# Performance work log

Measured on AMD Instinct MI355X. Metric: run time of the kernel, lower is better.

## Reference

```python
import jax, jax.numpy as jnp
import numpy as np

N_NODES = 100000
N_EDGES = 1000000
IN_F = 64
HEADS = 4
OUT_C = 32  # per-head channels
EDGE_DIM = 16
NEG_SLOPE = 0.2


def setup_inputs() -> dict:
    key = jax.random.key(0)
    ks = jax.random.split(key, 10)
    x = jax.random.normal(ks[0], (N_NODES, IN_F), dtype=jnp.float32)
    edge_index = jax.random.randint(ks[1], (2, N_EDGES), 0, N_NODES, dtype=jnp.int64)
    edge_attr = jax.random.normal(ks[2], (N_EDGES, EDGE_DIM), dtype=jnp.float32)
    s = 1.0 / np.sqrt(IN_F)
    W = jax.random.normal(ks[3], (IN_F, HEADS * OUT_C), dtype=jnp.float32) * s
    W_edge = jax.random.normal(ks[4], (EDGE_DIM, HEADS * OUT_C), dtype=jnp.float32) * (1.0 / np.sqrt(EDGE_DIM))
    att_src = jax.random.normal(ks[5], (HEADS, OUT_C), dtype=jnp.float32) * (1.0 / np.sqrt(OUT_C))
    att_dst = jax.random.normal(ks[6], (HEADS, OUT_C), dtype=jnp.float32) * (1.0 / np.sqrt(OUT_C))
    att_edge = jax.random.normal(ks[7], (HEADS, OUT_C), dtype=jnp.float32) * (1.0 / np.sqrt(OUT_C))
    bias = jnp.zeros((HEADS * OUT_C,), dtype=jnp.float32)
    return {"x": x, "edge_index": edge_index, "edge_attr": edge_attr,
            "W": W, "W_edge": W_edge, "att_src": att_src, "att_dst": att_dst,
            "att_edge": att_edge, "bias": bias}


def reference(x, edge_index, edge_attr, W, W_edge, att_src, att_dst, att_edge, bias):
    # PyG GATConv with edge_dim, add_self_loops=False, concat=True.
    N = x.shape[0]
    src = edge_index[0]  # message source j
    dst = edge_index[1]  # message target i

    x_proj = (x @ W).reshape(N, HEADS, OUT_C)          # [N,H,C]
    a_src = jnp.einsum('nhc,hc->nh', x_proj, att_src)  # [N,H]
    a_dst = jnp.einsum('nhc,hc->nh', x_proj, att_dst)  # [N,H]

    e_proj = (edge_attr @ W_edge).reshape(-1, HEADS, OUT_C)  # [E,H,C]
    a_edge = jnp.einsum('ehc,hc->eh', e_proj, att_edge)      # [E,H]

    alpha = a_src[src] + a_dst[dst] + a_edge                 # [E,H]
    alpha = jax.nn.leaky_relu(alpha, NEG_SLOPE)

    # edge softmax grouped by destination node
    seg_max = jax.ops.segment_max(alpha, dst, num_segments=N)  # [N,H]
    alpha = jnp.exp(alpha - seg_max[dst])
    denom = jax.ops.segment_sum(alpha, dst, num_segments=N)    # [N,H]
    alpha = alpha / (denom[dst] + 1e-16)

    msg = x_proj[src] * alpha[:, :, None]                      # [E,H,C]
    out = jax.ops.segment_sum(msg, dst, num_segments=N)        # [N,H,C]
    return out.reshape(N, HEADS * OUT_C) + bias
```

## Files before the change

kernel.cpp:

```cpp
#include <hip/hip_runtime.h>
#include <hip/hip_fp16.h>


#define HC 128
#define NEG 0.2f
#define NEG_INF (-3.0e38f)
#define CH 16

typedef __fp16 half2_t __attribute__((ext_vector_type(2)));

__device__ __forceinline__ unsigned short f2bf(float f) {
    unsigned u = __float_as_uint(f);
    return (unsigned short)((u + 0x7fffu + ((u >> 16) & 1u)) >> 16);
}
__device__ __forceinline__ unsigned pk_h2(float lo, float hi) {
    half2_t p = __builtin_amdgcn_cvt_pkrtz(lo, hi);
    union { half2_t h; unsigned u; } cv;
    cv.h = p;
    return cv.u;
}
__device__ __forceinline__ float h2f_bits(unsigned short bits) {
    __half_raw hr; hr.x = bits;
    return __half2float(*reinterpret_cast<__half*>(&hr));
}
__device__ __forceinline__ long ld_idx(const int* __restrict__ ei, long i, int m64) {
    return m64 ? (long)(((const long long*)ei)[i]) : (long)ei[i];
}
__device__ __forceinline__ int detect_m64(const int* __restrict__ ei, int* s_m64) {
    int t = threadIdx.x;
    if (t < 64) {
        unsigned long long bal = __ballot(ei[2 * t + 1] != 0);
        if (t == 0) *s_m64 = (bal == 0ull) ? 1 : 0;
    }
    __syncthreads();
    return *s_m64;
}

__global__ __launch_bounds__(256) void k_proj_hist(
    const float* __restrict__ x, const float* __restrict__ W,
    const float* __restrict__ as_, const float* __restrict__ ad_,
    const float* __restrict__ We, const float* __restrict__ ae,
    const float* __restrict__ eattr,
    unsigned short* __restrict__ xp, float* __restrict__ a_src,
    float* __restrict__ a_dst, const int* __restrict__ ei,
    int* __restrict__ deg, int* __restrict__ rank, uint2* __restrict__ aeh,
    int N, int E, int Nh) {
    __shared__ float x_s[64][68];
    __shared__ float q_s[64];
    __shared__ int s_m64;
    int t = threadIdx.x;
    int id = blockIdx.x;

    bool hist_role = (id < 2 * Nh) && (id & 1);
    if (hist_role) {
        int hid = id >> 1;
        int m64 = detect_m64(ei, &s_m64);
        if (t < 64) {
            int dd = t >> 2, h = t & 3;
            float s = 0.f;
            for (int c = 0; c < 32; ++c)
                s += We[dd * HC + h * 32 + c] * ae[h * 32 + c];
            q_s[t] = s;
        }
        __syncthreads();
        int base = hid * 1024 + t;
#pragma unroll
        for (int k = 0; k < 4; ++k) {
            int e = base + k * 256;
            if (e >= E) continue;
            long d = ld_idx(ei, (long)E + e, m64);
            const float4* pe = reinterpret_cast<const float4*>(eattr + (long)e * 16);
            float4 e0 = pe[0], e1 = pe[1], e2 = pe[2], e3 = pe[3];
            float ev[16] = {e0.x, e0.y, e0.z, e0.w, e1.x, e1.y, e1.z, e1.w,
                            e2.x, e2.y, e2.z, e2.w, e3.x, e3.y, e3.z, e3.w};
            float ov[4];
#pragma unroll
            for (int h = 0; h < 4; ++h) {
                float aev = 0.f;
#pragma unroll
                for (int dd = 0; dd < 16; ++dd) aev += ev[dd] * q_s[dd * 4 + h];
                ov[h] = aev;
            }
            aeh[e] = make_uint2(pk_h2(ov[0], ov[1]), pk_h2(ov[2], ov[3]));
            rank[e] = atomicAdd(&deg[d], 1);
        }
        return;
    }

    int pid = (id < 2 * Nh) ? (id >> 1) : (id - Nh);
    int n0 = pid * 64;
#pragma unroll
    for (int i = 0; i < 4; ++i) {
        int fl = i * 256 + t;
        int node = fl >> 4, f4 = fl & 15;
        float4 v = make_float4(0.f, 0.f, 0.f, 0.f);
        if (n0 + node < N)
            v = *reinterpret_cast<const float4*>(&x[(long)(n0 + node) * 64 + f4 * 4]);
        x_s[f4 * 4 + 0][node] = v.x;
        x_s[f4 * 4 + 1][node] = v.y;
        x_s[f4 * 4 + 2][node] = v.z;
        x_s[f4 * 4 + 3][node] = v.w;
    }
    __syncthreads();

    int c = t & 31;
    int nd = t >> 5;
    const float4* __restrict__ W4 = reinterpret_cast<const float4*>(W);
    float acc[8][4];
#pragma unroll
    for (int i = 0; i < 8; ++i)
#pragma unroll
        for (int j = 0; j < 4; ++j) acc[i][j] = 0.f;

#pragma unroll 8
    for (int k = 0; k < 64; ++k) {
        float4 w4 = W4[k * 32 + c];
        float4 xa = *reinterpret_cast<const float4*>(&x_s[k][nd * 8]);
        float4 xb = *reinterpret_cast<const float4*>(&x_s[k][nd * 8 + 4]);
        float xv[8] = {xa.x, xa.y, xa.z, xa.w, xb.x, xb.y, xb.z, xb.w};
#pragma unroll
        for (int i = 0; i < 8; ++i) {
            acc[i][0] += xv[i] * w4.x;
            acc[i][1] += xv[i] * w4.y;
            acc[i][2] += xv[i] * w4.z;
            acc[i][3] += xv[i] * w4.w;
        }
    }

    float4 s4 = *reinterpret_cast<const float4*>(&as_[c * 4]);
    float4 d4 = *reinterpret_cast<const float4*>(&ad_[c * 4]);
#pragma unroll
    for (int i = 0; i < 8; ++i) {
        int node = n0 + nd * 8 + i;
        if (node < N) {
            ushort4 o;
            o.x = f2bf(acc[i][0]); o.y = f2bf(acc[i][1]);
            o.z = f2bf(acc[i][2]); o.w = f2bf(acc[i][3]);
            *reinterpret_cast<ushort4*>(&xp[(long)node * HC + c * 4]) = o;
        }
        float ps = acc[i][0] * s4.x + acc[i][1] * s4.y + acc[i][2] * s4.z + acc[i][3] * s4.w;
        float pd = acc[i][0] * d4.x + acc[i][1] * d4.y + acc[i][2] * d4.z + acc[i][3] * d4.w;
#pragma unroll
        for (int off = 1; off < 8; off <<= 1) {
            ps += __shfl_xor(ps, off, 64);
            pd += __shfl_xor(pd, off, 64);
        }
        if ((c & 7) == 0 && node < N) {
            int h = c >> 3;
            a_src[(long)node * 4 + h] = ps;
            a_dst[(long)node * 4 + h] = pd;
        }
    }
}

__global__ __launch_bounds__(256) void k_scan1(
    const int* __restrict__ deg, int* __restrict__ row, int* __restrict__ bsum,
    int N) {
    __shared__ int s[256];
    int b = blockIdx.x, t = threadIdx.x;
    int base = b * 1024 + t * 4;
    int v[4], sum = 0;
#pragma unroll
    for (int i = 0; i < 4; ++i) {
        int idx = base + i;
        v[i] = (idx < N) ? deg[idx] : 0;
        sum += v[i];
    }
    s[t] = sum;
    __syncthreads();
    for (int off = 1; off < 256; off <<= 1) {
        int xv = (t >= off) ? s[t - off] : 0;
        __syncthreads();
        s[t] += xv;
        __syncthreads();
    }
    int run = s[t] - sum;
#pragma unroll
    for (int i = 0; i < 4; ++i) {
        int idx = base + i;
        if (idx < N) row[idx] = run;
        run += v[i];
    }
    if (t == 255) bsum[b] = s[255];
}

__global__ void k_scan2(int* __restrict__ bsum, int nb) {
    int t = threadIdx.x;
    if (t >= 64) return;
    int i0 = 2 * t, i1 = 2 * t + 1;
    int v0 = (i0 < nb) ? bsum[i0] : 0;
    int v1 = (i1 < nb) ? bsum[i1] : 0;
    int s = v0 + v1;
#pragma unroll
    for (int off = 1; off < 64; off <<= 1) {
        int u = __shfl_up(s, off, 64);
        if (t >= off) s += u;
    }
    int ex = s - (v0 + v1);
    if (i0 < nb) bsum[i0] = ex;
    if (i1 < nb) bsum[i1] = ex + v0;
}

__global__ __launch_bounds__(256) void k_place(
    const int* __restrict__ ei, const uint2* __restrict__ aeh,
    const int* __restrict__ rank, const float* __restrict__ a_src,
    const int* __restrict__ row, const int* __restrict__ bsum,
    uint4* __restrict__ srt, int E) {
    __shared__ int s_m64;
    int m64 = detect_m64(ei, &s_m64);
    int base = blockIdx.x * 512 + threadIdx.x;
#pragma unroll
    for (int k = 0; k < 2; ++k) {
        int e = base + k * 256;
        if (e >= E) continue;
        long s = ld_idx(ei, e, m64);
        long d = ld_idx(ei, (long)E + e, m64);
        uint2 av = aeh[e];
        int r = rank[e];
        float4 s4 = *reinterpret_cast<const float4*>(a_src + s * 4);
        float l0 = s4.x + h2f_bits((unsigned short)(av.x & 0xffffu));
        float l1 = s4.y + h2f_bits((unsigned short)(av.x >> 16));
        float l2 = s4.z + h2f_bits((unsigned short)(av.y & 0xffffu));
        float l3 = s4.w + h2f_bits((unsigned short)(av.y >> 16));
        int pos = row[d] + bsum[(int)(d >> 10)] + r;
        srt[pos] = make_uint4((unsigned)s, pk_h2(l0, l1), pk_h2(l2, l3), 0u);
    }
}

__global__ __launch_bounds__(128) void k_gather(
    const int* __restrict__ row, const int* __restrict__ bsum,
    const uint4* __restrict__ srt, const float* __restrict__ a_dst,
    const char* __restrict__ xpc, const float* __restrict__ bias,
    float* __restrict__ out, int N, int E) {
    int wid = threadIdx.x >> 6;
    int lane = threadIdx.x & 63;
    int n = blockIdx.x * 2 + wid;
    if (n >= N) return;
    int beg = row[n] + bsum[n >> 10];
    int end = (n + 1 < N) ? (row[n + 1] + bsum[(n + 1) >> 10]) : E;
    int h_s = lane & 3, e_s = lane >> 2;
    int par = lane >> 5;
    int cl = lane & 31;
    int h_a = cl >> 3;
    float adv = a_dst[(long)n * 4 + h_s];
    float m = NEG_INF, l = 0.f;
    float acc[4] = {0.f, 0.f, 0.f, 0.f};

    __shared__ float s_ex[2][CH][4];
    __shared__ int s_off[2][CH];
    __shared__ float s_bc[2][8];

    for (int cs = beg; cs < end; cs += CH) {
        int cnt = end - cs;
        if (cnt > CH) cnt = CH;
        float a = NEG_INF;
        if (e_s < cnt) {
            uint4 r = srt[cs + e_s];
            if (h_s == 0) s_off[wid][e_s] = (int)(r.x << 8);
            unsigned pr = (h_s & 2) ? r.z : r.y;
            unsigned bits = (h_s & 1) ? (pr >> 16) : (pr & 0xffffu);
            float v = h2f_bits((unsigned short)bits) + adv;
            a = (v > 0.f) ? v : NEG * v;
        }
        float cm = a;
        cm = fmaxf(cm, __shfl_xor(cm, 4, 64));
        cm = fmaxf(cm, __shfl_xor(cm, 8, 64));
        cm = fmaxf(cm, __shfl_xor(cm, 16, 64));
        cm = fmaxf(cm, __shfl_xor(cm, 32, 64));
        float nm = fmaxf(m, cm);
        float ex = (e_s < cnt) ? __expf(a - nm) : 0.f;
        s_ex[wid][e_s][h_s] = ex;
        float se = ex;
        se += __shfl_xor(se, 4, 64);
        se += __shfl_xor(se, 8, 64);
        se += __shfl_xor(se, 16, 64);
        se += __shfl_xor(se, 32, 64);
        float sc = __expf(m - nm);
        l = l * sc + se;
        m = nm;
        if (lane < 4) s_bc[wid][h_s] = sc;
        float scl = s_bc[wid][h_a];
        acc[0] *= scl; acc[1] *= scl; acc[2] *= scl; acc[3] *= scl;
        int j = 0;
        for (; j + 4 <= cnt; j += 4) {
            int ea0 = j + par, ea1 = j + 2 + par;
            int o0 = s_off[wid][ea0], o1 = s_off[wid][ea1];
            float w0 = s_ex[wid][ea0][h_a], w1 = s_ex[wid][ea1][h_a];
            uint2 v0 = *reinterpret_cast<const uint2*>(xpc + o0 + cl * 8);
            uint2 v1 = *reinterpret_cast<const uint2*>(xpc + o1 + cl * 8);
            acc[0] += w0 * __uint_as_float(v0.x << 16);
            acc[1] += w0 * __uint_as_float(v0.x & 0xffff0000u);
            acc[2] += w0 * __uint_as_float(v0.y << 16);
            acc[3] += w0 * __uint_as_float(v0.y & 0xffff0000u);
            acc[0] += w1 * __uint_as_float(v1.x << 16);
            acc[1] += w1 * __uint_as_float(v1.x & 0xffff0000u);
            acc[2] += w1 * __uint_as_float(v1.y << 16);
            acc[3] += w1 * __uint_as_float(v1.y & 0xffff0000u);
        }
        for (; j < cnt; j += 2) {
            int e = j + par;
            bool act = e < cnt;
            int o = s_off[wid][act ? e : j];
            float w = act ? s_ex[wid][e][h_a] : 0.f;
            uint2 v = *reinterpret_cast<const uint2*>(xpc + o + cl * 8);
            acc[0] += w * __uint_as_float(v.x << 16);
            acc[1] += w * __uint_as_float(v.x & 0xffff0000u);
            acc[2] += w * __uint_as_float(v.y << 16);
            acc[3] += w * __uint_as_float(v.y & 0xffff0000u);
        }
    }
    if (lane < 4) s_bc[wid][4 + h_s] = l;
#pragma unroll
    for (int k = 0; k < 4; ++k) acc[k] += __shfl_xor(acc[k], 32, 64);
    if (par == 0) {
        float d = s_bc[wid][4 + h_a] + 1e-16f;
        float4 b4 = *reinterpret_cast<const float4*>(bias + cl * 4);
        float4 o;
        o.x = acc[0] / d + b4.x;
        o.y = acc[1] / d + b4.y;
        o.z = acc[2] / d + b4.z;
        o.w = acc[3] / d + b4.w;
        *reinterpret_cast<float4*>(out + (long)n * HC + cl * 4) = o;
    }
}

extern "C" void kernel_launch(void* const* d_in, const int* in_sizes, int n_in,
                              void* d_out, int out_size, void* d_ws, size_t ws_size,
                              hipStream_t stream) {
    const float* x    = (const float*)d_in[0];
    const int*   ei   = (const int*)d_in[1];
    const float* ea   = (const float*)d_in[2];
    const float* W    = (const float*)d_in[3];
    const float* We   = (const float*)d_in[4];
    const float* as_  = (const float*)d_in[5];
    const float* ad_  = (const float*)d_in[6];
    const float* ae   = (const float*)d_in[7];
    const float* bias = (const float*)d_in[8];
    float* out = (float*)d_out;

    int N = in_sizes[0] / 64;
    int E = in_sizes[1] / 2;

    char* ws = (char*)d_ws;
    size_t off = 0;
    auto take = [&](size_t bytes) -> char* {
        char* p = ws + off;
        off += (bytes + 511) & ~(size_t)511;
        return p;
    };
    unsigned short* xp = (unsigned short*)take((size_t)N * HC * 2);
    float* a_src   = (float*)take((size_t)N * 4 * 4);
    float* a_dst   = (float*)take((size_t)N * 4 * 4);
    uint4* srt     = (uint4*)take((size_t)E * 16);
    uint2* aeh     = (uint2*)take((size_t)E * 8);
    int* rank      = (int*)take((size_t)E * 4);
    int* row       = (int*)take((size_t)(N + 1) * 4);
    int* bsum      = (int*)take(4096 * 4);
    int* deg       = (int*)take((size_t)N * 4);

    int Np = (N + 63) / 64;
    int Nh = (E + 1023) / 1024;
    int nblk = (N + 1023) / 1024;

    (void)hipMemsetAsync(deg, 0, (size_t)N * 4, stream);
    hipLaunchKernelGGL(k_proj_hist, dim3(Np + Nh), dim3(256), 0, stream,
                       x, W, as_, ad_, We, ae, ea, xp, a_src, a_dst,
                       ei, deg, rank, aeh, N, E, Nh);
    hipLaunchKernelGGL(k_scan1, dim3(nblk), dim3(256), 0, stream, deg, row, bsum, N);
    hipLaunchKernelGGL(k_scan2, dim3(1), dim3(64), 0, stream, bsum, nblk);
    hipLaunchKernelGGL(k_place, dim3((E + 511) / 512), dim3(256), 0, stream,
                       ei, aeh, rank, a_src, row, bsum, srt, E);
    hipLaunchKernelGGL(k_gather, dim3((N + 1) / 2), dim3(128), 0, stream,
                       row, bsum, srt, a_dst, (const char*)xp, bias, out, N, E);
}
```

Baseline: 274.0 us.

## Split fused projection/histogram kernel into separate hist and proj launches

```diff
diff --git a/kernel.cpp b/kernel.cpp
--- a/kernel.cpp
+++ b/kernel.cpp
@@ -36,59 +36,65 @@
     return *s_m64;
 }
 
-__global__ __launch_bounds__(256) void k_proj_hist(
-    const float* __restrict__ x, const float* __restrict__ W,
-    const float* __restrict__ as_, const float* __restrict__ ad_,
+__global__ __launch_bounds__(256) void k_hist(
     const float* __restrict__ We, const float* __restrict__ ae,
-    const float* __restrict__ eattr,
-    unsigned short* __restrict__ xp, float* __restrict__ a_src,
-    float* __restrict__ a_dst, const int* __restrict__ ei,
+    const float* __restrict__ eattr, const int* __restrict__ ei,
     int* __restrict__ deg, int* __restrict__ rank, uint2* __restrict__ aeh,
-    int N, int E, int Nh) {
-    __shared__ float x_s[64][68];
+    int E) {
     __shared__ float q_s[64];
     __shared__ int s_m64;
     int t = threadIdx.x;
-    int id = blockIdx.x;
-
-    bool hist_role = (id < 2 * Nh) && (id & 1);
-    if (hist_role) {
-        int hid = id >> 1;
-        int m64 = detect_m64(ei, &s_m64);
-        if (t < 64) {
-            int dd = t >> 2, h = t & 3;
-            float s = 0.f;
-            for (int c = 0; c < 32; ++c)
-                s += We[dd * HC + h * 32 + c] * ae[h * 32 + c];
-            q_s[t] = s;
-        }
-        __syncthreads();
-        int base = hid * 1024 + t;
-#pragma unroll
-        for (int k = 0; k < 4; ++k) {
-            int e = base + k * 256;
-            if (e >= E) continue;
-            long d = ld_idx(ei, (long)E + e, m64);
-            const float4* pe = reinterpret_cast<const float4*>(eattr + (long)e * 16);
-            float4 e0 = pe[0], e1 = pe[1], e2 = pe[2], e3 = pe[3];
-            float ev[16] = {e0.x, e0.y, e0.z, e0.w, e1.x, e1.y, e1.z, e1.w,
-                            e2.x, e2.y, e2.z, e2.w, e3.x, e3.y, e3.z, e3.w};
-            float ov[4];
-#pragma unroll
-            for (int h = 0; h < 4; ++h) {
-                float aev = 0.f;
-#pragma unroll
-                for (int dd = 0; dd < 16; ++dd) aev += ev[dd] * q_s[dd * 4 + h];
-                ov[h] = aev;
-            }
-            aeh[e] = make_uint2(pk_h2(ov[0], ov[1]), pk_h2(ov[2], ov[3]));
-            rank[e] = atomicAdd(&deg[d], 1);
-        }
-        return;
-    }
-
-    int pid = (id < 2 * Nh) ? (id >> 1) : (id - Nh);
-    int n0 = pid * 64;
+    int m64 = detect_m64(ei, &s_m64);
+    if (t < 64) {
+        int dd = t >> 2, h = t & 3;
+        float s = 0.f;
+        for (int c = 0; c < 32; ++c)
+            s += We[dd * HC + h * 32 + c] * ae[h * 32 + c];
+        q_s[t] = s;
+    }
+    __syncthreads();
+
+    int base = blockIdx.x * 512 + t;
+    int e0 = base, e1 = base + 256;
+    bool v0 = e0 < E, v1 = e1 < E;
+
+    long d0 = 0, d1 = 0;
+    if (v0) d0 = ld_idx(ei, (long)E + e0, m64);
+    if (v1) d1 = ld_idx(ei, (long)E + e1, m64);
+    int r0 = 0, r1 = 0;
+    if (v0) r0 = atomicAdd(&deg[d0], 1);
+    if (v1) r1 = atomicAdd(&deg[d1], 1);
+
+#pragma unroll
+    for (int k = 0; k < 2; ++k) {
+        int e = k ? e1 : e0;
+        bool v = k ? v1 : v0;
+        if (!v) continue;
+        const float4* pe = reinterpret_cast<const float4*>(eattr + (long)e * 16);
+        float4 ea0 = pe[0], ea1 = pe[1], ea2 = pe[2], ea3 = pe[3];
+        float ev[16] = {ea0.x, ea0.y, ea0.z, ea0.w, ea1.x, ea1.y, ea1.z, ea1.w,
+                        ea2.x, ea2.y, ea2.z, ea2.w, ea3.x, ea3.y, ea3.z, ea3.w};
+        float ov[4];
+#pragma unroll
+        for (int h = 0; h < 4; ++h) {
+            float aev = 0.f;
+#pragma unroll
+            for (int dd = 0; dd < 16; ++dd) aev += ev[dd] * q_s[dd * 4 + h];
+            ov[h] = aev;
+        }
+        aeh[e] = make_uint2(pk_h2(ov[0], ov[1]), pk_h2(ov[2], ov[3]));
+        rank[e] = k ? r1 : r0;
+    }
+}
+
+__global__ __launch_bounds__(256) void k_proj(
+    const float* __restrict__ x, const float* __restrict__ W,
+    const float* __restrict__ as_, const float* __restrict__ ad_,
+    unsigned short* __restrict__ xp, float* __restrict__ a_src,
+    float* __restrict__ a_dst, int N) {
+    __shared__ float x_s[64][68];
+    int t = threadIdx.x;
+    int n0 = blockIdx.x * 64;
 #pragma unroll
     for (int i = 0; i < 4; ++i) {
         int fl = i * 256 + t;
@@ -359,13 +365,13 @@
     int* deg       = (int*)take((size_t)N * 4);
 
     int Np = (N + 63) / 64;
-    int Nh = (E + 1023) / 1024;
     int nblk = (N + 1023) / 1024;
 
     (void)hipMemsetAsync(deg, 0, (size_t)N * 4, stream);
-    hipLaunchKernelGGL(k_proj_hist, dim3(Np + Nh), dim3(256), 0, stream,
-                       x, W, as_, ad_, We, ae, ea, xp, a_src, a_dst,
-                       ei, deg, rank, aeh, N, E, Nh);
+    hipLaunchKernelGGL(k_hist, dim3((E + 511) / 512), dim3(256), 0, stream,
+                       We, ae, ea, ei, deg, rank, aeh, E);
+    hipLaunchKernelGGL(k_proj, dim3(Np), dim3(256), 0, stream,
+                       x, W, as_, ad_, xp, a_src, a_dst, N);
     hipLaunchKernelGGL(k_scan1, dim3(nblk), dim3(256), 0, stream, deg, row, bsum, N);
     hipLaunchKernelGGL(k_scan2, dim3(1), dim3(64), 0, stream, bsum, nblk);
     hipLaunchKernelGGL(k_place, dim3((E + 511) / 512), dim3(256), 0, stream,
```

Measured after the change: 298.1 us. +8.8%, slower.
